# Performance work log

Hardware: AMD Instinct MI355X
Metric: run time of the kernel (lower is better)

The kernel has to match this reference:

```python
import jax, jax.numpy as jnp
import numpy as np

DIM = 768
HEADS = 12
HEAD_DIM = DIM // HEADS
SCALE = HEAD_DIM ** -0.5


def setup_inputs() -> dict:
    key = jax.random.key(0)
    k1, k2, k3, k4 = jax.random.split(key, 4)
    x = jax.random.normal(k1, (8, 1025, DIM), dtype=jnp.float32)
    # torch nn.Linear weight layout: (out_features, in_features)
    w_qkv = jax.random.normal(k2, (3 * DIM, DIM), dtype=jnp.float32) * (DIM ** -0.5)
    w_proj = jax.random.normal(k3, (DIM, DIM), dtype=jnp.float32) * (DIM ** -0.5)
    b_proj = jax.random.normal(k4, (DIM,), dtype=jnp.float32) * 0.01
    return {"x": x, "w_qkv": w_qkv, "w_proj": w_proj, "b_proj": b_proj}


def reference(x, w_qkv, w_proj, b_proj):
    B, N, C = x.shape
    H, D = HEADS, HEAD_DIM
    # qkv: (B, N, 3C) -> (3, B, H, N, D)
    qkv = jnp.einsum('bnc,oc->bno', x, w_qkv)
    qkv = qkv.reshape(B, N, 3, H, D).transpose(2, 0, 3, 1, 4)
    q, k, v = qkv[0], qkv[1], qkv[2]
    attn = jnp.einsum('bhnd,bhmd->bhnm', q, k) * SCALE
    attn = jax.nn.softmax(attn, axis=-1)
    out = jnp.einsum('bhnm,bhmd->bhnd', attn, v)
    out = out.transpose(0, 2, 1, 3).reshape(B, N, C)
    out = jnp.einsum('bnc,oc->bno', out, w_proj) + b_proj
    return out
```

## Files before the change

kernel.cpp:

```cpp
#include <hip/hip_runtime.h>
#include <stdint.h>

#define DIMC 768
#define NSEQ 1025
#define BATCH 8
#define HEADS 12
#define HDIM 64
#define OC3 2304
#define MROWS (BATCH * NSEQ)
#define NBH (BATCH * HEADS)
#define KVB 64
#define NT 17
#define QTILE 128
#define NQT 9
#define C2 0.1803368801111244f
#define OFFB (-11.541560327111707f)

typedef short bf16x8 __attribute__((ext_vector_type(8)));
typedef float f32x4 __attribute__((ext_vector_type(4)));
typedef float f32x16 __attribute__((ext_vector_type(16)));
typedef uint32_t u32x4 __attribute__((ext_vector_type(4)));

__device__ __forceinline__ uint32_t f2bf(float x) {
    uint32_t u = __builtin_bit_cast(uint32_t, x);
    return (u + 0x7fffu + ((u >> 16) & 1u)) >> 16;
}
__device__ __forceinline__ float4 ld4(const float* p) {
    return *reinterpret_cast<const float4*>(p);
}
__device__ __forceinline__ uint32_t cvtpk(float lo, float hi) {
    uint32_t r;
    asm("v_cvt_pk_bf16_f32 %0, %1, %2" : "=v"(r) : "v"(lo), "v"(hi));
    return r;
}
__device__ __forceinline__ void plswap(uint32_t& x, uint32_t& y) {
    asm volatile("v_permlane32_swap_b32 %0, %1" : "+v"(x), "+v"(y));
}
__device__ __forceinline__ void async_cp16(void* lds, const void* g) {
    __builtin_amdgcn_global_load_lds(
        (const __attribute__((address_space(1))) uint32_t*)g,
        (__attribute__((address_space(3))) uint32_t*)lds, 16, 0, 0);
}

__global__ __launch_bounds__(256) void cvt_all(const float* __restrict__ x,
                                               const float* __restrict__ wq,
                                               const float* __restrict__ wp,
                                               uint16_t* __restrict__ xb,
                                               uint16_t* __restrict__ wqb,
                                               uint16_t* __restrict__ wpb) {
    const int NX = MROWS * DIMC / 8, NQ = OC3 * DIMC / 8, NP = DIMC * DIMC / 8;
    const int i = blockIdx.x * 256 + threadIdx.x;
    const float* src;
    uint16_t* dst;
    int off;
    if (i < NX)                { src = x;  dst = xb;  off = i; }
    else if (i < NX + NQ)      { src = wq; dst = wqb; off = i - NX; }
    else if (i < NX + NQ + NP) { src = wp; dst = wpb; off = i - NX - NQ; }
    else return;
    const float4 a = ld4(src + off * 8), b = ld4(src + off * 8 + 4);
    uint4 o;
    o.x = f2bf(a.x) | (f2bf(a.y) << 16);
    o.y = f2bf(a.z) | (f2bf(a.w) << 16);
    o.z = f2bf(b.x) | (f2bf(b.y) << 16);
    o.w = f2bf(b.z) | (f2bf(b.w) << 16);
    *reinterpret_cast<uint4*>(dst + off * 8) = o;
}

template <bool QKVOUT, bool BIAS>
__global__ __launch_bounds__(256) void gemm_bf16_nt(const uint16_t* __restrict__ A,
                                                    const uint16_t* __restrict__ W,
                                                    const float* __restrict__ bias,
                                                    void* __restrict__ Out,
                                                    uint16_t* __restrict__ qh,
                                                    uint16_t* __restrict__ kh,
                                                    uint16_t* __restrict__ vt,
                                                    int M, int N, int K) {
    __shared__ __align__(16) char smem[32768];
    char* const As = smem;
    char* const Ws = smem + 16384;

    const int tid = threadIdx.x;
    const int wave = tid >> 6, lane = tid & 63;
    const int l15 = lane & 15, l4 = lane >> 4;
    const int wr = wave >> 1, wc = wave & 1;
    const int m0 = blockIdx.y * 128, n0 = blockIdx.x * 128;

    f32x4 acc[4][4] = {};

    int srow[4], scol[4];
#pragma unroll
    for (int i = 0; i < 4; ++i) {
        const int X = i * 4096 + wave * 1024 + lane * 16;
        const int row = X >> 7;
        const int slot = (X & 127) >> 4;
        srow[i] = row;
        scol[i] = (slot ^ (row & 7)) << 3;
    }

    for (int kt = 0; kt < K; kt += 64) {
        __syncthreads();
#pragma unroll
        for (int i = 0; i < 4; ++i) {
            int am = m0 + srow[i];
            if (am >= M) am = M - 1;
            async_cp16(As + i * 4096 + wave * 1024,
                       A + (size_t)am * K + kt + scol[i]);
            const int wn = n0 + srow[i];
            async_cp16(Ws + i * 4096 + wave * 1024,
                       W + (size_t)wn * K + kt + scol[i]);
        }
        __syncthreads();

#pragma unroll
        for (int ch = 0; ch < 2; ++ch) {
            const int kb = (ch << 6) + (l4 << 4);
            bf16x8 af[4], bw[4];
#pragma unroll
            for (int mi = 0; mi < 4; ++mi) {
                const int row = wr * 64 + mi * 16 + l15;
                af[mi] = *(const bf16x8*)(As + (row << 7) + (kb ^ ((row & 7) << 4)));
            }
#pragma unroll
            for (int nj = 0; nj < 4; ++nj) {
                const int row = wc * 64 + nj * 16 + l15;
                bw[nj] = *(const bf16x8*)(Ws + (row << 7) + (kb ^ ((row & 7) << 4)));
            }
#pragma unroll
            for (int mi = 0; mi < 4; ++mi)
#pragma unroll
                for (int nj = 0; nj < 4; ++nj)
                    acc[mi][nj] = __builtin_amdgcn_mfma_f32_16x16x32_bf16(
                        af[mi], bw[nj], acc[mi][nj], 0, 0, 0);
        }
    }

#pragma unroll
    for (int mi = 0; mi < 4; ++mi) {
#pragma unroll
        for (int r = 0; r < 4; ++r) {
            const int m = m0 + wr * 64 + mi * 16 + l4 * 4 + r;
            if (m < M) {
                if (QKVOUT) {
                    const int bidx = m / NSEQ;
                    const int nq = m - bidx * NSEQ;
#pragma unroll
                    for (int nj = 0; nj < 4; ++nj) {
                        const int n = n0 + wc * 64 + nj * 16 + l15;
                        const uint16_t v = (uint16_t)f2bf(acc[mi][nj][r]);
                        const int part = n / DIMC;
                        const int hh = (n - part * DIMC) >> 6;
                        const int dd = n & 63;
                        const size_t bh = (size_t)bidx * HEADS + hh;
                        if (part == 0)
                            qh[(bh * NSEQ + nq) * HDIM + dd] = v;
                        else if (part == 1)
                            kh[(bh * NSEQ + nq) * HDIM + dd] = v;
                        else
                            vt[(bh * HDIM + dd) * NSEQ + nq] = v;
                    }
                } else {
#pragma unroll
                    for (int nj = 0; nj < 4; ++nj) {
                        const int n = n0 + wc * 64 + nj * 16 + l15;
                        float v = acc[mi][nj][r];
                        if (BIAS) v += bias[n];
                        ((float*)Out)[(size_t)m * N + n] = v;
                    }
                }
            }
        }
    }
}

__global__ __launch_bounds__(256) void flash_attn2(const uint16_t* __restrict__ qh,
                                                   const uint16_t* __restrict__ kh,
                                                   const uint16_t* __restrict__ vt,
                                                   uint16_t* __restrict__ out) {
    const int wg = blockIdx.x;
    const int lg = (wg & 7) * 108 + (wg >> 3);
    const int qt = lg % NQT;
    const int bh = lg / NQT;
    const int h = bh % HEADS, b = bh / HEADS;

    const int tid = threadIdx.x;
    const int wave = tid >> 6, lane = tid & 63;
    const int l31 = lane & 31, lh = lane >> 5;

    __shared__ __align__(16) char smem[32768];

    const uint16_t* Kh = kh + (size_t)bh * NSEQ * HDIM;
    const uint16_t* Vt = vt + (size_t)bh * HDIM * NSEQ;

    bf16x8 qf[4];
    {
        int qrow = qt * QTILE + wave * 32 + l31;
        if (qrow > NSEQ - 1) qrow = NSEQ - 1;
        const uint16_t* Qg = qh + ((size_t)bh * NSEQ + qrow) * HDIM;
#pragma unroll
        for (int ds = 0; ds < 4; ++ds)
            qf[ds] = *(const bf16x8*)(Qg + ds * 16 + lh * 8);
    }

    bf16x8 ones;
#pragma unroll
    for (int i = 0; i < 8; ++i) ones[i] = (short)0x3F80;

    auto stageK = [&](int kv0, char* Kb) {
#pragma unroll
        for (int i = 0; i < 2; ++i) {
            const int X = i * 4096 + wave * 1024 + lane * 16;
            const int row = X >> 7;
            const int slot = (X & 127) >> 4;
            int kvg = kv0 + row;
            if (kvg > NSEQ - 1) kvg = NSEQ - 1;
            async_cp16(Kb + i * 4096 + wave * 1024,
                       Kh + (size_t)kvg * HDIM + ((slot ^ (row & 7)) << 3));
        }
    };
    auto stageV = [&](int kv0, char* Vb) {
#pragma unroll
        for (int i = 0; i < 2; ++i) {
            const int X = i * 4096 + wave * 1024 + lane * 16;
            const int d = X >> 7;
            const int slot = (X & 127) >> 4;
            async_cp16(Vb + i * 4096 + wave * 1024,
                       Vt + (size_t)d * NSEQ + kv0 + ((slot ^ (d & 7)) << 3));
        }
    };

    stageK(0, smem);
    stageV(0, smem + 16384);
    __syncthreads();

    f32x16 o[2] = {};
    f32x16 osum = {};

    for (int t = 0; t < NT; ++t) {
        const int cur = t & 1;
        const int kv0 = t * KVB;
        char* const Kc = smem + cur * 8192;
        char* const Vc = smem + 16384 + cur * 8192;

        if (t < NT - 1) {
            stageK(kv0 + KVB, smem + (cur ^ 1) * 8192);
            stageV(kv0 + KVB, smem + 16384 + (cur ^ 1) * 8192);
        }

        f32x16 s[2] = {};
        __builtin_amdgcn_s_setprio(1);
#pragma unroll
        for (int kvb = 0; kvb < 2; ++kvb) {
            const int krow = kvb * 32 + l31;
            const int kbase = (krow << 7);
            const int sw = (l31 & 7) << 4;
#pragma unroll
            for (int ds = 0; ds < 4; ++ds) {
                bf16x8 kf = *(const bf16x8*)(Kc + kbase + ((ds * 32 + lh * 16) ^ sw));
                s[kvb] = __builtin_amdgcn_mfma_f32_32x32x16_bf16(kf, qf[ds], s[kvb], 0, 0, 0);
            }
        }
        __builtin_amdgcn_s_setprio(0);

        if (t == NT - 1) {
#pragma unroll
            for (int kvb = 0; kvb < 2; ++kvb)
#pragma unroll
                for (int r = 0; r < 16; ++r) {
                    const int kvg = kv0 + kvb * 32 + (r & 3) + 8 * (r >> 2) + 4 * lh;
                    if (kvg >= NSEQ) s[kvb][r] = -INFINITY;
                }
        }

#pragma unroll
        for (int kvb = 0; kvb < 2; ++kvb)
#pragma unroll
            for (int r = 0; r < 16; ++r)
                s[kvb][r] = __builtin_amdgcn_exp2f(fmaf(s[kvb][r], C2, OFFB));

        bf16x8 pa[4];
#pragma unroll
        for (int kb = 0; kb < 4; ++kb) {
            const f32x16 S = s[kb >> 1];
            const int c = (kb & 1) * 8;
            uint32_t w0 = cvtpk(S[c + 0], S[c + 1]);
            uint32_t w2 = cvtpk(S[c + 4], S[c + 5]);
            plswap(w0, w2);
            uint32_t w1 = cvtpk(S[c + 2], S[c + 3]);
            uint32_t w3 = cvtpk(S[c + 6], S[c + 7]);
            plswap(w1, w3);
            u32x4 w;
            w[0] = w0; w[1] = w1; w[2] = w2; w[3] = w3;
            pa[kb] = __builtin_bit_cast(bf16x8, w);
        }

        __builtin_amdgcn_s_setprio(1);
#pragma unroll
        for (int kb = 0; kb < 4; ++kb)
            osum = __builtin_amdgcn_mfma_f32_32x32x16_bf16(ones, pa[kb], osum, 0, 0, 0);
#pragma unroll
        for (int db = 0; db < 2; ++db) {
            const int d = db * 32 + l31;
            const int dbase = (d << 7);
            const int sw = (l31 & 7) << 4;
#pragma unroll
            for (int kb = 0; kb < 4; ++kb) {
                bf16x8 vf = *(const bf16x8*)(Vc + dbase + ((kb * 32 + lh * 16) ^ sw));
                o[db] = __builtin_amdgcn_mfma_f32_32x32x16_bf16(vf, pa[kb], o[db], 0, 0, 0);
            }
        }
        __builtin_amdgcn_s_setprio(0);

        if (t < NT - 1) __syncthreads();
    }

    {
        const int qrow = qt * QTILE + wave * 32 + l31;
        if (qrow < NSEQ) {
            const float inv = 1.0f / osum[0];
            uint16_t* orow = out + (size_t)(b * NSEQ + qrow) * DIMC + h * HDIM;
#pragma unroll
            for (int db = 0; db < 2; ++db)
#pragma unroll
                for (int g = 0; g < 4; ++g) {
                    const int d = db * 32 + g * 8 + lh * 4;
                    uint2 ww;
                    ww.x = cvtpk(o[db][g * 4 + 0] * inv, o[db][g * 4 + 1] * inv);
                    ww.y = cvtpk(o[db][g * 4 + 2] * inv, o[db][g * 4 + 3] * inv);
                    *(uint2*)(orow + d) = ww;
                }
        }
    }
}

extern "C" void kernel_launch(void* const* d_in, const int* in_sizes, int n_in,
                              void* d_out, int out_size, void* d_ws, size_t ws_size,
                              hipStream_t stream) {
    const float* x      = (const float*)d_in[0];
    const float* w_qkv  = (const float*)d_in[1];
    const float* w_proj = (const float*)d_in[2];
    const float* b_proj = (const float*)d_in[3];
    float* out = (float*)d_out;

    const size_t NHD = (size_t)NBH * NSEQ * HDIM;
    uint16_t* xb   = (uint16_t*)d_ws;
    uint16_t* wqb  = xb  + (size_t)MROWS * DIMC;
    uint16_t* wpb  = wqb + (size_t)OC3 * DIMC;
    uint16_t* qh   = wpb + (size_t)DIMC * DIMC;
    uint16_t* kh   = qh + NHD;
    uint16_t* vt   = kh + NHD;
    uint16_t* attb = vt + NHD;

    const dim3 blk(256);
    const int ncvt = (MROWS * DIMC + OC3 * DIMC + DIMC * DIMC) / 8;
    cvt_all<<<dim3((ncvt + 255) / 256), blk, 0, stream>>>(x, w_qkv, w_proj, xb, wqb, wpb);

    gemm_bf16_nt<true, false><<<dim3(OC3 / 128, (MROWS + 127) / 128), blk, 0, stream>>>(
        xb, wqb, nullptr, nullptr, qh, kh, vt, MROWS, OC3, DIMC);

    flash_attn2<<<dim3(NQT * HEADS * BATCH), blk, 0, stream>>>(qh, kh, vt, attb);

    gemm_bf16_nt<false, true><<<dim3(DIMC / 128, (MROWS + 127) / 128), blk, 0, stream>>>(
        attb, wpb, b_proj, out, nullptr, nullptr, nullptr, MROWS, DIMC, DIMC);
}
```

Before: 139.7 us.

## Write V row-major from QKV GEMM and transpose in a separate padded kernel

The QKV GEMM epilogue used to scatter V directly into a transposed layout, which produced strided 2-byte global writes. It now stores V in the same row-major per-head layout as Q and K. A new LDS-based transpose kernel then writes V^T with a padded stride of 17*64, so attention V loads stay 16-byte aligned and never read past the sequence end. The cost is an extra kernel launch and an extra read and write of V, plus more workspace.

```diff
diff --git a/kernel.cpp b/kernel.cpp
--- a/kernel.cpp
+++ b/kernel.cpp
@@ -13,6 +13,7 @@
 #define NT 17
 #define QTILE 128
 #define NQT 9
+#define VSTRIDE (NT * KVB)
 #define C2 0.1803368801111244f
 #define OFFB (-11.541560327111707f)
 
@@ -73,7 +74,7 @@
                                                     void* __restrict__ Out,
                                                     uint16_t* __restrict__ qh,
                                                     uint16_t* __restrict__ kh,
-                                                    uint16_t* __restrict__ vt,
+                                                    uint16_t* __restrict__ vh,
                                                     int M, int N, int K) {
     __shared__ __align__(16) char smem[32768];
     char* const As = smem;
@@ -150,13 +151,8 @@
                         const int part = n / DIMC;
                         const int hh = (n - part * DIMC) >> 6;
                         const int dd = n & 63;
-                        const size_t bh = (size_t)bidx * HEADS + hh;
-                        if (part == 0)
-                            qh[(bh * NSEQ + nq) * HDIM + dd] = v;
-                        else if (part == 1)
-                            kh[(bh * NSEQ + nq) * HDIM + dd] = v;
-                        else
-                            vt[(bh * HDIM + dd) * NSEQ + nq] = v;
+                        uint16_t* dst = (part == 0) ? qh : (part == 1) ? kh : vh;
+                        dst[(((size_t)bidx * HEADS + hh) * NSEQ + nq) * HDIM + dd] = v;
                     }
                 } else {
 #pragma unroll
@@ -169,6 +165,45 @@
                 }
             }
         }
+    }
+}
+
+__global__ __launch_bounds__(256) void transpose_v(const uint16_t* __restrict__ vh,
+                                                   uint16_t* __restrict__ vt) {
+    const int kt = blockIdx.x, bh = blockIdx.y;
+    __shared__ __align__(16) char lds[8192];
+    const int tid = threadIdx.x;
+    const uint16_t* src = vh + (size_t)bh * NSEQ * HDIM;
+    uint16_t* dst = vt + (size_t)bh * HDIM * VSTRIDE + kt * KVB;
+
+#pragma unroll
+    for (int i = 0; i < 2; ++i) {
+        const int s = i * 256 + tid;
+        const int kv = s >> 3, c = s & 7;
+        int kvg = kt * KVB + kv;
+        if (kvg > NSEQ - 1) kvg = NSEQ - 1;
+        const uint4 d4 = *(const uint4*)(src + (size_t)kvg * HDIM + c * 8);
+        *(uint4*)(lds + (kv << 7) + ((c ^ (kv & 7)) << 4)) = d4;
+    }
+    __syncthreads();
+
+#pragma unroll
+    for (int i = 0; i < 2; ++i) {
+        const int s = i * 256 + tid;
+        const int d = s >> 3, c = s & 7;
+        uint32_t w[4];
+#pragma unroll
+        for (int p = 0; p < 4; ++p) {
+            const int k0 = c * 8 + p * 2, k1 = k0 + 1;
+            const uint32_t lo = *(const uint16_t*)(lds + (k0 << 7) +
+                ((((d >> 3) ^ (k0 & 7)) << 4) + ((d & 7) << 1)));
+            const uint32_t hi = *(const uint16_t*)(lds + (k1 << 7) +
+                ((((d >> 3) ^ (k1 & 7)) << 4) + ((d & 7) << 1)));
+            w[p] = lo | (hi << 16);
+        }
+        uint4 o4;
+        o4.x = w[0]; o4.y = w[1]; o4.z = w[2]; o4.w = w[3];
+        *(uint4*)(dst + (size_t)d * VSTRIDE + c * 8) = o4;
     }
 }
 
@@ -189,7 +224,7 @@
     __shared__ __align__(16) char smem[32768];
 
     const uint16_t* Kh = kh + (size_t)bh * NSEQ * HDIM;
-    const uint16_t* Vt = vt + (size_t)bh * HDIM * NSEQ;
+    const uint16_t* Vt = vt + (size_t)bh * HDIM * VSTRIDE;
 
     bf16x8 qf[4];
     {
@@ -224,7 +259,7 @@
             const int d = X >> 7;
             const int slot = (X & 127) >> 4;
             async_cp16(Vb + i * 4096 + wave * 1024,
-                       Vt + (size_t)d * NSEQ + kv0 + ((slot ^ (d & 7)) << 3));
+                       Vt + (size_t)d * VSTRIDE + kv0 + ((slot ^ (d & 7)) << 3));
         }
     };
 
@@ -342,20 +377,24 @@
     float* out = (float*)d_out;
 
     const size_t NHD = (size_t)NBH * NSEQ * HDIM;
+    const size_t NVT = (size_t)NBH * HDIM * VSTRIDE;
     uint16_t* xb   = (uint16_t*)d_ws;
     uint16_t* wqb  = xb  + (size_t)MROWS * DIMC;
     uint16_t* wpb  = wqb + (size_t)OC3 * DIMC;
     uint16_t* qh   = wpb + (size_t)DIMC * DIMC;
     uint16_t* kh   = qh + NHD;
-    uint16_t* vt   = kh + NHD;
-    uint16_t* attb = vt + NHD;
+    uint16_t* vh   = kh + NHD;
+    uint16_t* vt   = vh + NHD;
+    uint16_t* attb = vt + NVT;
 
     const dim3 blk(256);
     const int ncvt = (MROWS * DIMC + OC3 * DIMC + DIMC * DIMC) / 8;
     cvt_all<<<dim3((ncvt + 255) / 256), blk, 0, stream>>>(x, w_qkv, w_proj, xb, wqb, wpb);
 
     gemm_bf16_nt<true, false><<<dim3(OC3 / 128, (MROWS + 127) / 128), blk, 0, stream>>>(
-        xb, wqb, nullptr, nullptr, qh, kh, vt, MROWS, OC3, DIMC);
+        xb, wqb, nullptr, nullptr, qh, kh, vh, MROWS, OC3, DIMC);
+
+    transpose_v<<<dim3(NT, NBH), blk, 0, stream>>>(vh, vt);
 
     flash_attn2<<<dim3(NQT * HEADS * BATCH), blk, 0, stream>>>(qh, kh, vt, attb);
 
```

New measurement: 140.8 us. No clear change (+0.8%).
